# Kernel optimization log

Measured on AMD Instinct MI355X. Metric: run time of the kernel, lower is better.

The kernel has to match this reference:

```python
import jax, jax.numpy as jnp
import numpy as np

DELTA_PULL = 0.5
DELTA_PUSH = 1.5
EPS = 1e-6


def setup_inputs() -> dict:
    key = jax.random.key(0)
    k1, k2 = jax.random.split(key)
    B, C, H, W, K = 4, 16, 512, 512, 16
    embedding_maps = jax.random.normal(k1, (B, C, H, W), dtype=jnp.float32)
    instance_masks = jax.random.randint(k2, (B, K, H, W), 0, 2, dtype=jnp.int32)
    return {"embedding_maps": embedding_maps, "instance_masks": instance_masks}


def reference(embedding_maps, instance_masks):
    emb = embedding_maps                      # [B, C, H, W]
    m = (instance_masks > 0).astype(emb.dtype)  # [B, K, H, W]
    K = m.shape[1]

    # per-instance masked segment reductions over all H*W pixels
    counts = m.sum((-1, -2))                                   # [B, K]
    sums = jnp.einsum('bchw,bkhw->bkc', emb, m)                # [B, K, C]
    sq_sums = jnp.einsum('bchw,bkhw->bkc', emb * emb, m)       # [B, K, C]

    valid = counts > 0                                          # [B, K]
    safe_counts = jnp.maximum(counts, 1.0)
    means = sums / safe_counts[..., None]                       # [B, K, C] exact fg mean

    # sum over fg pixels of ||e - mean||^2 = sq_sum - 2*mean.sum + n*mean^2
    pull_k = (sq_sums - 2.0 * means * sums + counts[..., None] * means * means).sum(-1)
    pull_k = jnp.where(valid, pull_k / (counts + EPS), 0.0)     # [B, K]

    M = valid.sum(-1).astype(emb.dtype)                         # [B] num valid instances
    pull_b = pull_k.sum(-1) / jnp.maximum(M, 1.0)               # [B]

    # pairwise push between valid instance means (i < j)
    diff = means[:, :, None, :] - means[:, None, :, :]          # [B, K, K, C]
    dist = jnp.sqrt((diff * diff).sum(-1) + 1e-12)              # [B, K, K]
    iu = jnp.arange(K)
    pair = valid[:, :, None] & valid[:, None, :] & (iu[:, None] < iu[None, :])
    push_terms = jnp.where(pair, jnp.maximum(DELTA_PUSH - dist, 0.0) ** 2, 0.0)
    npairs = M * (M - 1.0) / 2.0
    push_b = jnp.where(M > 1.0, push_terms.sum((-1, -2)) / jnp.maximum(npairs, 1.0), 0.0)

    return (DELTA_PULL * pull_b + push_b).mean()
```

## Files before the change

kernel.cpp:

```cpp
#include <hip/hip_runtime.h>

#define BB 4
#define CC 16
#define KK 16
#define HWP (512 * 512)
#define TPB 1024
#define TPW 256
#define NTILES (HWP / TPB)
#define THREADS 256
#define NGROUP (TPW / 32)
#define NSLICE 16
#define WSTOT (64 + 1024 + 1024)

typedef short bf16x8 __attribute__((ext_vector_type(8)));
typedef float f32x4 __attribute__((ext_vector_type(4)));

__device__ __forceinline__ float fmaxf_(float a, float b) { return a > b ? a : b; }

__device__ __forceinline__ unsigned short f2bf(float f) {
    unsigned u = __float_as_uint(f);
    u += 0x7FFFu + ((u >> 16) & 1u);
    return (unsigned short)(u >> 16);
}
__device__ __forceinline__ unsigned pkbf(float x, float y) {
    return (unsigned)f2bf(x) | ((unsigned)f2bf(y) << 16);
}
__device__ __forceinline__ unsigned pkmask(int a, int b) {
    unsigned ua = (a > 0) ? 1u : 0u;
    unsigned ub = (b > 0) ? 1u : 0u;
    return (ua | (ub << 16)) * 0x3F80u;
}

__global__ __launch_bounds__(THREADS) void disc_mfma_kernel(
    const float* __restrict__ emb, const int* __restrict__ masks,
    float* __restrict__ ws)
{
    __shared__ float redbuf[4][64][9];
    __shared__ float cnt_red[4][16];

    const int tid = threadIdx.x;
    const int lane = tid & 63;
    const int wave = tid >> 6;
    const int b = blockIdx.x / NTILES;
    const int tile = blockIdx.x % NTILES;
    const size_t base_px = (size_t)tile * TPB + wave * TPW;

    const int quad = lane >> 4;
    const int r = lane & 15;

    const int*   mp = masks + ((size_t)b * KK + r) * HWP + base_px + quad * 8;
    const float* ep = emb   + ((size_t)b * CC + r) * HWP + base_px + quad * 8;

    union { bf16x8 v; unsigned short s[8]; } Bones;
    #pragma unroll
    for (int i = 0; i < 8; ++i) Bones.s[i] = 0x3F80;

    f32x4 acc_s = {0.f, 0.f, 0.f, 0.f};
    f32x4 acc_q = {0.f, 0.f, 0.f, 0.f};
    f32x4 acc_c = {0.f, 0.f, 0.f, 0.f};

    int4 m0c = ((const int4*)mp)[0], m1c = ((const int4*)mp)[1];
    float4 e0c = ((const float4*)ep)[0], e1c = ((const float4*)ep)[1];

    #pragma unroll
    for (int g = 0; g < NGROUP; ++g) {
        int4 m0n, m1n; float4 e0n, e1n;
        if (g + 1 < NGROUP) {
            const int*   mpn = mp + (g + 1) * 32;
            const float* epn = ep + (g + 1) * 32;
            m0n = ((const int4*)mpn)[0]; m1n = ((const int4*)mpn)[1];
            e0n = ((const float4*)epn)[0]; e1n = ((const float4*)epn)[1];
        }
#if __has_builtin(__builtin_amdgcn_sched_barrier)
        __builtin_amdgcn_sched_barrier(0);
#endif
        union { bf16x8 v; unsigned u[4]; } A;
        A.u[0] = pkmask(m0c.x, m0c.y);
        A.u[1] = pkmask(m0c.z, m0c.w);
        A.u[2] = pkmask(m1c.x, m1c.y);
        A.u[3] = pkmask(m1c.z, m1c.w);

        union { bf16x8 v; unsigned u[4]; } Bf, B2;
        Bf.u[0] = pkbf(e0c.x, e0c.y);
        Bf.u[1] = pkbf(e0c.z, e0c.w);
        Bf.u[2] = pkbf(e1c.x, e1c.y);
        Bf.u[3] = pkbf(e1c.z, e1c.w);
        B2.u[0] = pkbf(e0c.x * e0c.x, e0c.y * e0c.y);
        B2.u[1] = pkbf(e0c.z * e0c.z, e0c.w * e0c.w);
        B2.u[2] = pkbf(e1c.x * e1c.x, e1c.y * e1c.y);
        B2.u[3] = pkbf(e1c.z * e1c.z, e1c.w * e1c.w);

        acc_s = __builtin_amdgcn_mfma_f32_16x16x32_bf16(A.v, Bf.v, acc_s, 0, 0, 0);
        acc_q = __builtin_amdgcn_mfma_f32_16x16x32_bf16(A.v, B2.v, acc_q, 0, 0, 0);
        acc_c = __builtin_amdgcn_mfma_f32_16x16x32_bf16(A.v, Bones.v, acc_c, 0, 0, 0);

        if (g + 1 < NGROUP) { m0c = m0n; m1c = m1n; e0c = e0n; e1c = e1n; }
    }

    #pragma unroll
    for (int j = 0; j < 4; ++j) {
        redbuf[wave][lane][j] = acc_s[j];
        redbuf[wave][lane][4 + j] = acc_q[j];
    }
    if (r == 0) {
        #pragma unroll
        for (int reg = 0; reg < 4; ++reg) cnt_red[wave][quad * 4 + reg] = acc_c[reg];
    }
    __syncthreads();

    float* slice = ws + (size_t)(blockIdx.x & (NSLICE - 1)) * WSTOT;
    #pragma unroll
    for (int t = 0; t < 2; ++t) {
        const int fi = tid + t * THREADS;
        const int l2 = fi >> 3, j = fi & 7;
        float v = redbuf[0][l2][j] + redbuf[1][l2][j]
                + redbuf[2][l2][j] + redbuf[3][l2][j];
        const int reg = j & 3, isq = j >> 2;
        const int krow = (l2 >> 4) * 4 + reg;
        const int ccol = l2 & 15;
        atomicAdd(&slice[64 + isq * 1024 + ((size_t)b * KK + krow) * CC + ccol], v);
    }
    if (tid < KK) {
        float ctot = cnt_red[0][tid] + cnt_red[1][tid] + cnt_red[2][tid] + cnt_red[3][tid];
        atomicAdd(&slice[b * KK + tid], ctot);
    }
}

__global__ __launch_bounds__(256) void disc_finalize_kernel(
    const float* __restrict__ ws, float* __restrict__ out)
{
    __shared__ float red[WSTOT];
    __shared__ float means[BB][KK][CC];
    __shared__ float partial[BB];
    const int tid = threadIdx.x;

    for (int idx = tid; idx < WSTOT; idx += 256) {
        float t = 0.f;
        #pragma unroll
        for (int s = 0; s < NSLICE; ++s) t += ws[(size_t)s * WSTOT + idx];
        red[idx] = t;
    }
    __syncthreads();

    const float* red_cnt = red;
    const float* red_sum = red + 64;
    const float* red_sq  = red + 64 + 1024;

    const int b = tid >> 6;
    const int lane = tid & 63;

    const float DELTA_PULL = 0.5f;
    const float DELTA_PUSH = 1.5f;
    const float EPS = 1e-6f;

    float cntk = 0.f;
    bool valid = false;
    float pull_k = 0.f;
    if (lane < KK) {
        int k = lane;
        cntk = red_cnt[b * KK + k];
        valid = cntk > 0.f;
        float safe = fmaxf_(cntk, 1.f);
        float acc_sq = 0.f, acc_ss = 0.f;
        #pragma unroll
        for (int c = 0; c < CC; ++c) {
            float sv = red_sum[(b * KK + k) * CC + c];
            means[b][k][c] = sv / safe;
            acc_sq += red_sq[(b * KK + k) * CC + c];
            acc_ss += sv * sv;
        }
        if (valid) pull_k = (acc_sq - acc_ss / cntk) / (cntk + EPS);
    }

    unsigned long long bal = __ballot(lane < KK && valid);
    float M = (float)__popcll(bal);

    float ps = pull_k;
    #pragma unroll
    for (int d = 32; d >= 1; d >>= 1) ps += __shfl_xor(ps, d, 64);
    float pull_b = ps / fmaxf_(M, 1.f);

    __syncthreads();

    float push = 0.f;
    for (int t = lane; t < KK * KK; t += 64) {
        int i = t >> 4, j = t & 15;
        if (i < j && ((bal >> i) & 1ull) && ((bal >> j) & 1ull)) {
            float d2 = 1e-12f;
            #pragma unroll
            for (int c = 0; c < CC; ++c) {
                float df = means[b][i][c] - means[b][j][c];
                d2 = fmaf(df, df, d2);
            }
            float dist = sqrtf(d2);
            float h = fmaxf_(DELTA_PUSH - dist, 0.f);
            push += h * h;
        }
    }
    #pragma unroll
    for (int d = 32; d >= 1; d >>= 1) push += __shfl_xor(push, d, 64);

    if (lane == 0) {
        float npairs = M * (M - 1.f) * 0.5f;
        float push_b = (M > 1.f) ? push / fmaxf_(npairs, 1.f) : 0.f;
        partial[b] = DELTA_PULL * pull_b + push_b;
    }
    __syncthreads();
    if (tid == 0) {
        out[0] = (partial[0] + partial[1] + partial[2] + partial[3]) * 0.25f;
    }
}

extern "C" void kernel_launch(void* const* d_in, const int* in_sizes, int n_in,
                              void* d_out, int out_size, void* d_ws, size_t ws_size,
                              hipStream_t stream) {
    const float* emb = (const float*)d_in[0];
    const int* masks = (const int*)d_in[1];
    float* ws = (float*)d_ws;

    hipMemsetAsync(d_ws, 0, NSLICE * WSTOT * sizeof(float), stream);

    dim3 grid(BB * NTILES);
    disc_mfma_kernel<<<grid, THREADS, 0, stream>>>(emb, masks, ws);
    disc_finalize_kernel<<<1, 256, 0, stream>>>(ws, (float*)d_out);
}
```

Measured before the change: 158.7 us.

## Bit-pack instance masks through LDS and build MFMA A fragments from bits

Each lane now loads contiguous int4 mask chunks for all 16 instances up front, packs them into 16-bit per-pixel membership words in shared memory, and then rebuilds the bf16 one-hot A operand by shifting and masking those bits. This replaces the strided per-row mask loads with fully coalesced row reads that can all be in flight at once. The explicit one-step software prefetch and sched_barrier on the embedding loads are removed, so overlap of those loads is left to the compiler. It adds an LDS round trip that stays within each wave, so no block barrier is needed, plus more live registers during the mask gather.

Result: faster. 155.4 us (-2.1%).

```diff
diff --git a/kernel.cpp b/kernel.cpp
--- a/kernel.cpp
+++ b/kernel.cpp
@@ -25,16 +25,12 @@
 __device__ __forceinline__ unsigned pkbf(float x, float y) {
     return (unsigned)f2bf(x) | ((unsigned)f2bf(y) << 16);
 }
-__device__ __forceinline__ unsigned pkmask(int a, int b) {
-    unsigned ua = (a > 0) ? 1u : 0u;
-    unsigned ub = (b > 0) ? 1u : 0u;
-    return (ua | (ub << 16)) * 0x3F80u;
-}
 
 __global__ __launch_bounds__(THREADS) void disc_mfma_kernel(
     const float* __restrict__ emb, const int* __restrict__ masks,
     float* __restrict__ ws)
 {
+    __shared__ __align__(16) unsigned short bits[TPB];
     __shared__ float redbuf[4][64][9];
     __shared__ float cnt_red[4][16];
 
@@ -48,53 +44,57 @@
     const int quad = lane >> 4;
     const int r = lane & 15;
 
-    const int*   mp = masks + ((size_t)b * KK + r) * HWP + base_px + quad * 8;
-    const float* ep = emb   + ((size_t)b * CC + r) * HWP + base_px + quad * 8;
+    const int* mbase = masks + (size_t)b * KK * HWP + base_px + 4 * lane;
+    unsigned v0 = 0, v1 = 0, v2 = 0, v3 = 0;
+    #pragma unroll
+    for (int k = 0; k < KK; ++k) {
+        int4 mm = *(const int4*)(mbase + (size_t)k * HWP);
+        v0 |= (mm.x > 0 ? 1u : 0u) << k;
+        v1 |= (mm.y > 0 ? 1u : 0u) << k;
+        v2 |= (mm.z > 0 ? 1u : 0u) << k;
+        v3 |= (mm.w > 0 ? 1u : 0u) << k;
+    }
+    uint2 pk;
+    pk.x = v0 | (v1 << 16);
+    pk.y = v2 | (v3 << 16);
+    ((uint2*)bits)[(wave * TPW) / 4 + lane] = pk;
 
     union { bf16x8 v; unsigned short s[8]; } Bones;
     #pragma unroll
     for (int i = 0; i < 8; ++i) Bones.s[i] = 0x3F80;
+
+    const float* ebase = emb + ((size_t)b * CC + r) * HWP + base_px;
 
     f32x4 acc_s = {0.f, 0.f, 0.f, 0.f};
     f32x4 acc_q = {0.f, 0.f, 0.f, 0.f};
     f32x4 acc_c = {0.f, 0.f, 0.f, 0.f};
 
-    int4 m0c = ((const int4*)mp)[0], m1c = ((const int4*)mp)[1];
-    float4 e0c = ((const float4*)ep)[0], e1c = ((const float4*)ep)[1];
-
     #pragma unroll
     for (int g = 0; g < NGROUP; ++g) {
-        int4 m0n, m1n; float4 e0n, e1n;
-        if (g + 1 < NGROUP) {
-            const int*   mpn = mp + (g + 1) * 32;
-            const float* epn = ep + (g + 1) * 32;
-            m0n = ((const int4*)mpn)[0]; m1n = ((const int4*)mpn)[1];
-            e0n = ((const float4*)epn)[0]; e1n = ((const float4*)epn)[1];
-        }
-#if __has_builtin(__builtin_amdgcn_sched_barrier)
-        __builtin_amdgcn_sched_barrier(0);
-#endif
+        const int p0 = wave * TPW + g * 32;
+
+        uint4 bw = *(const uint4*)&bits[p0 + quad * 8];
         union { bf16x8 v; unsigned u[4]; } A;
-        A.u[0] = pkmask(m0c.x, m0c.y);
-        A.u[1] = pkmask(m0c.z, m0c.w);
-        A.u[2] = pkmask(m1c.x, m1c.y);
-        A.u[3] = pkmask(m1c.z, m1c.w);
-
+        A.u[0] = ((bw.x >> r) & 0x00010001u) * 0x3F80u;
+        A.u[1] = ((bw.y >> r) & 0x00010001u) * 0x3F80u;
+        A.u[2] = ((bw.z >> r) & 0x00010001u) * 0x3F80u;
+        A.u[3] = ((bw.w >> r) & 0x00010001u) * 0x3F80u;
+
+        const float4* ep = (const float4*)(ebase + g * 32 + quad * 8);
+        float4 f0 = ep[0], f1 = ep[1];
         union { bf16x8 v; unsigned u[4]; } Bf, B2;
-        Bf.u[0] = pkbf(e0c.x, e0c.y);
-        Bf.u[1] = pkbf(e0c.z, e0c.w);
-        Bf.u[2] = pkbf(e1c.x, e1c.y);
-        Bf.u[3] = pkbf(e1c.z, e1c.w);
-        B2.u[0] = pkbf(e0c.x * e0c.x, e0c.y * e0c.y);
-        B2.u[1] = pkbf(e0c.z * e0c.z, e0c.w * e0c.w);
-        B2.u[2] = pkbf(e1c.x * e1c.x, e1c.y * e1c.y);
-        B2.u[3] = pkbf(e1c.z * e1c.z, e1c.w * e1c.w);
+        Bf.u[0] = pkbf(f0.x, f0.y);
+        Bf.u[1] = pkbf(f0.z, f0.w);
+        Bf.u[2] = pkbf(f1.x, f1.y);
+        Bf.u[3] = pkbf(f1.z, f1.w);
+        B2.u[0] = pkbf(f0.x * f0.x, f0.y * f0.y);
+        B2.u[1] = pkbf(f0.z * f0.z, f0.w * f0.w);
+        B2.u[2] = pkbf(f1.x * f1.x, f1.y * f1.y);
+        B2.u[3] = pkbf(f1.z * f1.z, f1.w * f1.w);
 
         acc_s = __builtin_amdgcn_mfma_f32_16x16x32_bf16(A.v, Bf.v, acc_s, 0, 0, 0);
         acc_q = __builtin_amdgcn_mfma_f32_16x16x32_bf16(A.v, B2.v, acc_q, 0, 0, 0);
         acc_c = __builtin_amdgcn_mfma_f32_16x16x32_bf16(A.v, Bones.v, acc_c, 0, 0, 0);
-
-        if (g + 1 < NGROUP) { m0c = m0n; m1c = m1n; e0c = e0n; e1c = e1n; }
     }
 
     #pragma unroll
```
